# Kernel tuning notes

Measured on AMD Instinct MI355X. Metric: run time of the kernel, lower is better.

## Reference

```python
import jax, jax.numpy as jnp
import numpy as np

X_DIM, Y_DIM = 16, 8
D_MODEL, N_HEADS, N_LAYERS = 256, 8, 8
D_HEAD = D_MODEL // N_HEADS            # 32 (hidden_out_size // n_heads)
D_FF = D_HEAD * 8 * N_HEADS            # 2048 (feed_forward_dimensions)
B, S_PAST, S_FUT = 4, 1024, 512
MIN_STD = 0.01
LN_EPS = 1e-5
ATTN_EPS = 1e-6


def setup_inputs() -> dict:
    key = jax.random.key(0)
    ks = jax.random.split(key, 24)
    def nrm(k, shape, s=0.02):
        return jax.random.normal(k, shape, jnp.float32) * s
    L, d, dff = N_LAYERS, D_MODEL, D_FF
    x_size = X_DIM + Y_DIM
    return {
        "past_x": jax.random.normal(ks[0], (B, S_PAST, X_DIM), jnp.float32),
        "past_y": jax.random.normal(ks[1], (B, S_PAST, Y_DIM), jnp.float32),
        "future_x": jax.random.normal(ks[2], (B, S_FUT, X_DIM), jnp.float32),
        "enc_W": nrm(ks[3], (x_size, d)), "enc_b": jnp.zeros((d,), jnp.float32),
        "Wq": nrm(ks[4], (L, d, d)), "bq": jnp.zeros((L, d), jnp.float32),
        "Wk": nrm(ks[5], (L, d, d)), "bk": jnp.zeros((L, d), jnp.float32),
        "Wv": nrm(ks[6], (L, d, d)), "bv": jnp.zeros((L, d), jnp.float32),
        "Wo": nrm(ks[7], (L, d, d)), "bo": jnp.zeros((L, d), jnp.float32),
        "ln1_w": jnp.ones((L, d), jnp.float32), "ln1_b": jnp.zeros((L, d), jnp.float32),
        "W1": nrm(ks[8], (L, d, dff)), "b1": jnp.zeros((L, dff), jnp.float32),
        "W2": nrm(ks[9], (L, dff, d)), "b2": jnp.zeros((L, d), jnp.float32),
        "ln2_w": jnp.ones((L, d), jnp.float32), "ln2_b": jnp.zeros((L, d), jnp.float32),
        "mean_W": nrm(ks[10], (d, Y_DIM)), "mean_b": jnp.zeros((Y_DIM,), jnp.float32),
        "std_W": nrm(ks[11], (d, Y_DIM)), "std_b": jnp.zeros((Y_DIM,), jnp.float32),
    }


def _ln(x, w, b):
    m = jnp.mean(x, axis=-1, keepdims=True)
    v = jnp.var(x, axis=-1, keepdims=True)
    return (x - m) * jax.lax.rsqrt(v + LN_EPS) * w + b


def _causal_linear_attn(q, k, v):
    # q,k,v: [B, N, H, D]; phi(x) = elu(x) + 1 (fast_transformers default feature map)
    q = jax.nn.elu(q) + 1.0
    k = jax.nn.elu(k) + 1.0
    # cumulative outer-product state S_i = sum_{j<=i} phi(k_j) v_j^T : [B,N,H,D,D]
    kv = jnp.cumsum(jnp.einsum('bnhd,bnhm->bnhdm', k, v), axis=1)
    num = jnp.einsum('bnhd,bnhdm->bnhm', q, kv)
    z = jnp.einsum('bnhd,bnhd->bnh', q, jnp.cumsum(k, axis=1))
    return num / (z[..., None] + ATTN_EPS)


def _forward(past_x, past_y, future_x, enc_W, enc_b, Wq, bq, Wk, bk, Wv, bv,
             Wo, bo, ln1_w, ln1_b, W1, b1, W2, b2, ln2_w, ln2_b,
             mean_W, mean_b, std_W, std_b):
    Bz, Sf = future_x.shape[0], future_x.shape[1]
    steps = past_y.shape[1]
    # future y placeholder = last observed y, repeated
    fy = jnp.repeat(past_y[:, -1:, :], Sf, axis=1)
    context = jnp.concatenate([past_x, past_y], axis=-1)
    target = jnp.concatenate([future_x, fy], axis=-1)
    x = jax.lax.stop_gradient(jnp.concatenate([context, target], axis=1))  # .detach()
    x = x @ enc_W + enc_b                      # [B, N, D_MODEL]
    N = x.shape[1]
    for i in range(N_LAYERS):
        q = (x @ Wq[i] + bq[i]).reshape(Bz, N, N_HEADS, D_HEAD)
        k = (x @ Wk[i] + bk[i]).reshape(Bz, N, N_HEADS, D_HEAD)
        v = (x @ Wv[i] + bv[i]).reshape(Bz, N, N_HEADS, D_HEAD)
        a = _causal_linear_attn(q, k, v).reshape(Bz, N, D_MODEL)
        x = _ln(x + (a @ Wo[i] + bo[i]), ln1_w[i], ln1_b[i])   # post-norm (fast_transformers)
        y = jax.nn.relu(x @ W1[i] + b1[i]) @ W2[i] + b2[i]
        x = _ln(x + y, ln2_w[i], ln2_b[i])
    out = x[:, steps:, :]                      # keep only the target segment
    mean = out @ mean_W + mean_b
    sigma = MIN_STD + (1.0 - MIN_STD) * jax.nn.softplus(out @ std_W + std_b)
    return mean, sigma


def reference(past_x, past_y, future_x, enc_W, enc_b, Wq, bq, Wk, bk, Wv, bv,
              Wo, bo, ln1_w, ln1_b, W1, b1, W2, b2, ln2_w, ln2_b,
              mean_W, mean_b, std_W, std_b):
    return _forward(past_x, past_y, future_x, enc_W, enc_b, Wq, bq, Wk, bk,
                    Wv, bv, Wo, bo, ln1_w, ln1_b, W1, b1, W2, b2,
                    ln2_w, ln2_b, mean_W, mean_b, std_W, std_b)
```

## Files before the change

### kernel.cpp

```cpp
#include <hip/hip_runtime.h>
#include <hip/hip_bf16.h>
#include <math.h>

#define BB 4
#define SP 1024
#define SF 512
#define NN 1536
#define DD 256
#define HH 8
#define DH 32
#define DFF 2048
#define LL 8
#define TOK (BB*NN)
#define NSEG 48
#define SEGLEN 32

typedef __attribute__((ext_vector_type(8))) short bf16x8;
typedef __attribute__((ext_vector_type(4))) float f32x4;
typedef __hip_bfloat16 bf16;

__device__ __forceinline__ void gld_lds16(const void* g, void* l) {
    __builtin_amdgcn_global_load_lds(
        (const __attribute__((address_space(1))) void*)g,
        (__attribute__((address_space(3))) void*)l, 16, 0, 0);
}

__global__ __launch_bounds__(256) void wtrans_kernel(
    const float* __restrict__ src, bf16* __restrict__ dst, int K, int N)
{
    __shared__ float tile[64][65];
    int k0 = blockIdx.x*64, n0 = blockIdx.y*64;
    const float* s = src + (size_t)blockIdx.z*K*N;
    bf16* d = dst + (size_t)blockIdx.z*K*N;
    int t = threadIdx.x, c = t & 63, r4 = t >> 6;
    #pragma unroll
    for (int rr = 0; rr < 64; rr += 4)
        tile[rr+r4][c] = s[(size_t)(k0+rr+r4)*N + n0 + c];
    __syncthreads();
    #pragma unroll
    for (int rr = 0; rr < 64; rr += 4) {
        int n = rr + r4;
        d[(size_t)(n0+n)*K + k0 + c] = __float2bfloat16(tile[c][n]);
    }
}

template<int BM, bool SPLITK, bool BOUT>
__device__ __forceinline__ void gemm_core(
    const bf16* __restrict__ A, const bf16* __restrict__ Wt,
    const float* __restrict__ bias, float* __restrict__ Cf,
    bf16* __restrict__ Cb, int N, int K, int epi, int kc0, int kc1)
{
    constexpr int MI = BM/32;
    __shared__ bf16 As[BM*64];
    __shared__ bf16 Bs[128*64];
    int tid = threadIdx.x, lane = tid & 63, wid = tid >> 6;
    int m0 = blockIdx.x*BM, n0 = blockIdx.y*128;
    int wm = (wid & 1)*(BM/2), wn = (wid >> 1)*64;

    f32x4 acc[MI][4] = {};

    int rA = wid*(BM/4) + (lane >> 3);
    int rB = wid*32 + (lane >> 3);
    int c_st = (lane & 7)*8;
    const bf16* Ag = A  + (size_t)(m0 + rA)*K + c_st;
    const bf16* Bg = Wt + (size_t)(n0 + rB)*K + c_st;
    bf16* Asw = As + (wid*(BM/4))*64;
    bf16* Bsw = Bs + (wid*32)*64;

    int a_off = (wm + (lane & 15))*64 + (lane >> 4)*8;
    int b_off = (wn + (lane & 15))*64 + (lane >> 4)*8;

    for (int kc = kc0; kc < kc1; kc += 64) {
        #pragma unroll
        for (int i = 0; i < MI; i++)
            gld_lds16(Ag + (size_t)(i*8)*K + kc, Asw + (i*8)*64);
        #pragma unroll
        for (int i = 0; i < 4; i++)
            gld_lds16(Bg + (size_t)(i*8)*K + kc, Bsw + (i*8)*64);
        __syncthreads();
        #pragma unroll
        for (int ks = 0; ks < 2; ks++) {
            bf16x8 af[MI], bfr[4];
            #pragma unroll
            for (int i = 0; i < MI; i++)
                af[i] = *(const bf16x8*)(As + a_off + i*16*64 + ks*32);
            #pragma unroll
            for (int j = 0; j < 4; j++)
                bfr[j] = *(const bf16x8*)(Bs + b_off + j*16*64 + ks*32);
            #pragma unroll
            for (int i = 0; i < MI; i++)
                #pragma unroll
                for (int j = 0; j < 4; j++)
                    acc[i][j] = __builtin_amdgcn_mfma_f32_16x16x32_bf16(
                        af[i], bfr[j], acc[i][j], 0, 0, 0);
        }
        __syncthreads();
    }

    if constexpr (BOUT) {
        bf16* Ct = Bs;
        #pragma unroll
        for (int j = 0; j < 4; j++) {
            int col = wn + j*16 + (lane & 15);
            float bv = bias[n0 + col];
            #pragma unroll
            for (int i = 0; i < MI; i++) {
                #pragma unroll
                for (int r = 0; r < 4; r++) {
                    int row = wm + i*16 + (lane >> 4)*4 + r;
                    float v = acc[i][j][r] + bv;
                    if (epi == 1) v = fmaxf(v, 0.f);
                    else if (epi == 2) v = (v > 0.f) ? v + 1.f : expf(v);
                    Ct[row*128 + (col ^ (((row >> 2) & 3) << 4))] = __float2bfloat16(v);
                }
            }
        }
        __syncthreads();
        #pragma unroll
        for (int u = 0; u < 4; u++) {
            int e = tid*32 + u*8;
            int row = e >> 7, c0 = e & 127;
            bf16x8 val = *(const bf16x8*)(Ct + row*128 + (c0 ^ (((row >> 2) & 3) << 4)));
            *(bf16x8*)(Cb + (size_t)(m0 + row)*N + n0 + c0) = val;
        }
    } else {
        int col_base = n0 + wn + (lane & 15);
        int row_base = m0 + wm + (lane >> 4)*4;
        #pragma unroll
        for (int j = 0; j < 4; j++) {
            int col = col_base + j*16;
            float bv = SPLITK ? 0.f : bias[col];
            #pragma unroll
            for (int i = 0; i < MI; i++) {
                #pragma unroll
                for (int r = 0; r < 4; r++) {
                    int row = row_base + i*16 + r;
                    if (SPLITK) {
                        unsafeAtomicAdd(&Cf[(size_t)row*N + col], acc[i][j][r]);
                    } else {
                        float v = acc[i][j][r] + bv;
                        if (epi == 1) v = fmaxf(v, 0.f);
                        else if (epi == 2) v = (v > 0.f) ? v + 1.f : expf(v);
                        if (Cb) Cb[(size_t)row*N + col] = __float2bfloat16(v);
                        else    Cf[(size_t)row*N + col] = v;
                    }
                }
            }
        }
    }
}

template<int BM, bool BOUT>
__global__ __launch_bounds__(256) void mfma_gemm_kernel(
    const bf16* __restrict__ A, const bf16* __restrict__ Wt,
    const float* __restrict__ bias, float* __restrict__ Cf,
    bf16* __restrict__ Cb, int N, int K, int epi)
{
    gemm_core<BM, false, BOUT>(A, Wt, bias, Cf, Cb, N, K, epi, 0, K);
}

template<int BM>
__global__ __launch_bounds__(256) void mfma_gemm_splitk_kernel(
    const bf16* __restrict__ A, const bf16* __restrict__ Wt,
    float* __restrict__ Cf, int N, int K, int KC)
{
    int kc0 = blockIdx.z*KC;
    gemm_core<BM, true, false>(A, Wt, nullptr, Cf, nullptr, N, K, 0, kc0, kc0 + KC);
}

template<int BM>
__global__ __launch_bounds__(256) void mfma_qkv_kernel(
    const bf16* __restrict__ Xb,
    const bf16* __restrict__ Wqt, const bf16* __restrict__ Wkt, const bf16* __restrict__ Wvt,
    const float* __restrict__ bq, const float* __restrict__ bk, const float* __restrict__ bv,
    float* __restrict__ Q, float* __restrict__ K, float* __restrict__ V, int layer)
{
    int z = blockIdx.z;
    const bf16* Wt = (z == 0) ? Wqt : (z == 1) ? Wkt : Wvt;
    const float* b = (z == 0) ? bq : (z == 1) ? bk : bv;
    float* C = (z == 0) ? Q : (z == 1) ? K : V;
    gemm_core<BM, false, false>(Xb, Wt + (size_t)layer*DD*DD, b + (size_t)layer*DD,
                                C, nullptr, DD, DD, (z == 2) ? 0 : 2, 0, DD);
}

__global__ __launch_bounds__(256) void encode_kernel(
    const float* __restrict__ px, const float* __restrict__ py,
    const float* __restrict__ fx, const float* __restrict__ encW,
    const float* __restrict__ encb, float* __restrict__ X, bf16* __restrict__ Xb)
{
    int tok = blockIdx.x;
    int t = threadIdx.x;
    int b = tok / NN, n = tok % NN;
    __shared__ float in[24];
    if (t < 16) {
        in[t] = (n < SP) ? px[((size_t)b*SP + n)*16 + t]
                         : fx[((size_t)b*SF + (n - SP))*16 + t];
    } else if (t < 24) {
        int j = t - 16;
        in[t] = (n < SP) ? py[((size_t)b*SP + n)*8 + j]
                         : py[((size_t)b*SP + (SP-1))*8 + j];
    }
    __syncthreads();
    float acc = encb[t];
    #pragma unroll
    for (int j = 0; j < 24; j++) acc = fmaf(in[j], encW[j*DD + t], acc);
    X[(size_t)tok*DD + t] = acc;
    Xb[(size_t)tok*DD + t] = __float2bfloat16(acc);
}

__global__ __launch_bounds__(256) void attnA_kernel(
    const float* __restrict__ K, const float* __restrict__ V,
    float* __restrict__ SegS, float* __restrict__ SegZ)
{
    int bid = blockIdx.x;
    int seg = bid % NSEG; int bh = bid / NSEG;
    int h = bh & 7, b = bh >> 3;
    int t = threadIdx.x;
    int d = t & 31, mg = t >> 5, m0 = mg*4;
    int tok0 = b*NN + seg*SEGLEN;
    const float* Kp = K + (size_t)tok0*DD + h*DH;
    const float* Vp = V + (size_t)tok0*DD + h*DH;
    float a0=0,a1=0,a2=0,a3=0, ks=0;
    #pragma unroll 4
    for (int i = 0; i < SEGLEN; i++) {
        float kd = Kp[(size_t)i*DD + d];
        float4 vv = *(const float4*)(Vp + (size_t)i*DD + m0);
        a0 = fmaf(kd, vv.x, a0); a1 = fmaf(kd, vv.y, a1);
        a2 = fmaf(kd, vv.z, a2); a3 = fmaf(kd, vv.w, a3);
        ks += kd;
    }
    float4 o = {a0, a1, a2, a3};
    *(float4*)(SegS + ((size_t)bid*32 + d)*32 + m0) = o;
    if (mg == 0) SegZ[(size_t)bid*32 + d] = ks;
}

__global__ __launch_bounds__(256) void attnA2_kernel(
    float* __restrict__ SegS, float* __restrict__ SegZ)
{
    int bh = blockIdx.x, y = blockIdx.y, t = threadIdx.x;
    int e = y*256 + t;
    float* p = SegS + (size_t)bh*NSEG*1024 + e;
    float v[NSEG];
    #pragma unroll
    for (int s = 0; s < NSEG; s++) v[s] = p[(size_t)s*1024];
    float run = 0.f;
    #pragma unroll
    for (int s = 0; s < NSEG; s++) {
        p[(size_t)s*1024] = run;
        run += v[s];
    }
    if (y == 0 && t < 32) {
        float* pz = SegZ + (size_t)bh*NSEG*32 + t;
        float vz[NSEG];
        #pragma unroll
        for (int s = 0; s < NSEG; s++) vz[s] = pz[(size_t)s*32];
        float runz = 0.f;
        #pragma unroll
        for (int s = 0; s < NSEG; s++) {
            pz[(size_t)s*32] = runz;
            runz += vz[s];
        }
    }
}

__global__ __launch_bounds__(256) void attnB_kernel(
    const float* __restrict__ Q, const float* __restrict__ K, const float* __restrict__ V,
    const float* __restrict__ SegS, const float* __restrict__ SegZ,
    bf16* __restrict__ A)
{
    int wid = threadIdx.x >> 6;
    int lane = threadIdx.x & 63;
    int bid = blockIdx.x*4 + wid;
    int seg = bid % NSEG; int bh = bid / NSEG;
    int h = bh & 7, b = bh >> 3;
    int m = lane & 31, dh = lane >> 5, dh16 = dh*16;
    int tok0 = b*NN + seg*SEGLEN;

    __shared__ float qs[4][SEGLEN][32], ksm[4][SEGLEN][32], vs[4][SEGLEN][32];
    const float* Qp = Q + (size_t)tok0*DD + h*DH;
    const float* Kp = K + (size_t)tok0*DD + h*DH;
    const float* Vp = V + (size_t)tok0*DD + h*DH;
    #pragma unroll
    for (int f = lane; f < SEGLEN*8; f += 64) {
        int r = f >> 3, c = (f & 7)*4;
        *(float4*)&qs[wid][r][c]  = *(const float4*)(Qp + (size_t)r*DD + c);
        *(float4*)&ksm[wid][r][c] = *(const float4*)(Kp + (size_t)r*DD + c);
        *(float4*)&vs[wid][r][c]  = *(const float4*)(Vp + (size_t)r*DD + c);
    }
    __syncthreads();

    float kv[16], kss[16];
    const float* Pp = SegS + (size_t)bid*1024;
    const float* Zp = SegZ + (size_t)bid*32;
    #pragma unroll
    for (int j = 0; j < 16; j++) {
        kv[j]  = Pp[(dh16 + j)*32 + m];
        kss[j] = Zp[dh16 + j];
    }

    bf16* Ap = A + (size_t)tok0*DD + h*DH;
    for (int i = 0; i < SEGLEN; i++) {
        float qv[16], kk[16];
        #pragma unroll
        for (int c = 0; c < 4; c++) {
            float4 t4 = *(const float4*)&qs[wid][i][dh16 + 4*c];
            qv[4*c] = t4.x; qv[4*c+1] = t4.y; qv[4*c+2] = t4.z; qv[4*c+3] = t4.w;
            float4 k4 = *(const float4*)&ksm[wid][i][dh16 + 4*c];
            kk[4*c] = k4.x; kk[4*c+1] = k4.y; kk[4*c+2] = k4.z; kk[4*c+3] = k4.w;
        }
        float vm = vs[wid][i][m];
        #pragma unroll
        for (int j = 0; j < 16; j++) {
            kv[j] = fmaf(kk[j], vm, kv[j]);
            kss[j] += kk[j];
        }
        float p0=0,p1=0,p2=0,p3=0,z0=0,z1=0,z2=0,z3=0;
        #pragma unroll
        for (int j = 0; j < 4; j++) {
            p0 = fmaf(qv[j],     kv[j],     p0);
            p1 = fmaf(qv[4+j],   kv[4+j],   p1);
            p2 = fmaf(qv[8+j],   kv[8+j],   p2);
            p3 = fmaf(qv[12+j],  kv[12+j],  p3);
            z0 = fmaf(qv[j],     kss[j],    z0);
            z1 = fmaf(qv[4+j],   kss[4+j],  z1);
            z2 = fmaf(qv[8+j],   kss[8+j],  z2);
            z3 = fmaf(qv[12+j],  kss[12+j], z3);
        }
        float nump = (p0+p1)+(p2+p3);
        float zp   = (z0+z1)+(z2+z3);
        nump += __shfl_xor(nump, 32, 64);
        zp   += __shfl_xor(zp,   32, 64);
        if (dh == 0) Ap[(size_t)i*DD + m] = __float2bfloat16(nump / (zp + 1e-6f));
    }
}

__global__ __launch_bounds__(256) void resid_ln_kernel(
    const float* __restrict__ Xin, const float* __restrict__ G,
    const float* __restrict__ gb,
    const float* __restrict__ w, const float* __restrict__ b,
    float* __restrict__ Xout, bf16* __restrict__ Xbout)
{
    int tok = blockIdx.x, t = threadIdx.x;
    size_t idx = (size_t)tok*DD + t;
    float v = Xin[idx] + G[idx] + (gb ? gb[t] : 0.f);
    float s = v, s2 = v*v;
    #pragma unroll
    for (int off = 32; off >= 1; off >>= 1) {
        s  += __shfl_xor(s,  off, 64);
        s2 += __shfl_xor(s2, off, 64);
    }
    __shared__ float ps[4], ps2[4];
    int wid = t >> 6;
    if ((t & 63) == 0) { ps[wid] = s; ps2[wid] = s2; }
    __syncthreads();
    float S  = ps[0] + ps[1] + ps[2] + ps[3];
    float S2 = ps2[0] + ps2[1] + ps2[2] + ps2[3];
    float mean = S * (1.f/256.f);
    float var  = S2 * (1.f/256.f) - mean*mean;
    float o = (v - mean) * rsqrtf(var + 1e-5f) * w[t] + b[t];
    Xout[idx] = o;
    Xbout[idx] = __float2bfloat16(o);
}

__global__ __launch_bounds__(256) void head_kernel(
    const float* __restrict__ X,
    const float* __restrict__ meanW, const float* __restrict__ meanB,
    const float* __restrict__ stdW,  const float* __restrict__ stdB,
    float* __restrict__ out)
{
    int wv = threadIdx.x >> 6;
    int lane = threadIdx.x & 63;
    int idx = blockIdx.x*4 + wv;
    int b = idx / SF, i = idx % SF;
    const float* row = X + ((size_t)(b*NN + SP + i))*DD;
    __shared__ float xs[4][DD];
    *(float4*)&xs[wv][lane*4] = *(const float4*)(row + lane*4);
    __syncthreads();

    int j = lane & 7;
    int which = (lane >> 3) & 1;
    int seg = lane >> 4;
    const float* W = which ? stdW : meanW;
    float p = 0.f;
    #pragma unroll 16
    for (int d = seg*64; d < seg*64 + 64; d++) p = fmaf(xs[wv][d], W[d*8 + j], p);
    p += __shfl_xor(p, 16, 64);
    p += __shfl_xor(p, 32, 64);
    if (lane < 16) {
        if (which == 0) {
            out[((size_t)b*SF + i)*8 + j] = p + meanB[j];
        } else {
            float s = p + stdB[j];
            float sp = fmaxf(s, 0.f) + log1pf(expf(-fabsf(s)));
            out[(size_t)BB*SF*8 + ((size_t)b*SF + i)*8 + j] = 0.01f + 0.99f*sp;
        }
    }
}

extern "C" void kernel_launch(void* const* d_in, const int* in_sizes, int n_in,
                              void* d_out, int out_size, void* d_ws, size_t ws_size,
                              hipStream_t stream)
{
    (void)in_sizes; (void)n_in; (void)out_size; (void)ws_size;
    const float* past_x   = (const float*)d_in[0];
    const float* past_y   = (const float*)d_in[1];
    const float* future_x = (const float*)d_in[2];
    const float* enc_W    = (const float*)d_in[3];
    const float* enc_b    = (const float*)d_in[4];
    const float* Wq       = (const float*)d_in[5];
    const float* bq       = (const float*)d_in[6];
    const float* Wk       = (const float*)d_in[7];
    const float* bk       = (const float*)d_in[8];
    const float* Wv       = (const float*)d_in[9];
    const float* bv       = (const float*)d_in[10];
    const float* Wo       = (const float*)d_in[11];
    const float* bo       = (const float*)d_in[12];
    const float* ln1_w    = (const float*)d_in[13];
    const float* ln1_b    = (const float*)d_in[14];
    const float* W1       = (const float*)d_in[15];
    const float* b1       = (const float*)d_in[16];
    const float* W2       = (const float*)d_in[17];
    const float* b2       = (const float*)d_in[18];
    const float* ln2_w    = (const float*)d_in[19];
    const float* ln2_b    = (const float*)d_in[20];
    const float* mean_W   = (const float*)d_in[21];
    const float* mean_b   = (const float*)d_in[22];
    const float* std_W    = (const float*)d_in[23];
    const float* std_b    = (const float*)d_in[24];
    float* out = (float*)d_out;

    char* base = (char*)d_ws;
    size_t off = 0;
    float* X  = (float*)(base + off); off += (size_t)TOK*DD*4;
    bf16* Xb  = (bf16*)(base + off);  off += (size_t)TOK*DD*2;
    bf16* Hb  = (bf16*)(base + off);  off += (size_t)TOK*DFF*2;
    float* Qb = (float*)Hb;
    float* Kb = Qb + (size_t)TOK*DD;
    float* Vb = Kb + (size_t)TOK*DD;
    bf16* Ab  = (bf16*)(base + off);  off += (size_t)TOK*DD*2;
    float* G  = (float*)(base + off); off += (size_t)TOK*DD*4;
    float* SegS = (float*)(base + off); off += (size_t)BB*HH*NSEG*1024*4;
    float* SegZ = (float*)(base + off); off += (size_t)BB*HH*NSEG*32*4;
    bf16* Wqt = (bf16*)(base + off); off += (size_t)LL*DD*DD*2;
    bf16* Wkt = (bf16*)(base + off); off += (size_t)LL*DD*DD*2;
    bf16* Wvt = (bf16*)(base + off); off += (size_t)LL*DD*DD*2;
    bf16* Wot = (bf16*)(base + off); off += (size_t)LL*DD*DD*2;
    bf16* W1t = (bf16*)(base + off); off += (size_t)LL*DD*DFF*2;
    bf16* W2t = (bf16*)(base + off); off += (size_t)LL*DFF*DD*2;

    wtrans_kernel<<<dim3(4, 4, LL),  256, 0, stream>>>(Wq, Wqt, DD, DD);
    wtrans_kernel<<<dim3(4, 4, LL),  256, 0, stream>>>(Wk, Wkt, DD, DD);
    wtrans_kernel<<<dim3(4, 4, LL),  256, 0, stream>>>(Wv, Wvt, DD, DD);
    wtrans_kernel<<<dim3(4, 4, LL),  256, 0, stream>>>(Wo, Wot, DD, DD);
    wtrans_kernel<<<dim3(4, 32, LL), 256, 0, stream>>>(W1, W1t, DD, DFF);
    wtrans_kernel<<<dim3(32, 4, LL), 256, 0, stream>>>(W2, W2t, DFF, DD);

    encode_kernel<<<TOK, 256, 0, stream>>>(past_x, past_y, future_x, enc_W, enc_b, X, Xb);

    for (int l = 0; l < LL; l++) {
        mfma_qkv_kernel<32><<<dim3(TOK/32, 2, 3), 256, 0, stream>>>(
            Xb, Wqt, Wkt, Wvt, bq, bk, bv, Qb, Kb, Vb, l);
        attnA_kernel<<<BB*HH*NSEG, 256, 0, stream>>>(Kb, Vb, SegS, SegZ);
        attnA2_kernel<<<dim3(BB*HH, 4), 256, 0, stream>>>(SegS, SegZ);
        attnB_kernel<<<BB*HH*NSEG/4, 256, 0, stream>>>(Qb, Kb, Vb, SegS, SegZ, Ab);
        mfma_gemm_kernel<32, false><<<dim3(TOK/32, 2), 256, 0, stream>>>(
            Ab, Wot + (size_t)l*DD*DD, bo + (size_t)l*DD, G, nullptr, DD, DD, 0);
        resid_ln_kernel<<<TOK, 256, 0, stream>>>(
            X, G, nullptr, ln1_w + l*DD, ln1_b + l*DD, X, Xb);
        mfma_gemm_kernel<64, true><<<dim3(TOK/64, DFF/128), 256, 0, stream>>>(
            Xb, W1t + (size_t)l*DD*DFF, b1 + (size_t)l*DFF, nullptr, Hb, DFF, DD, 1);
        hipMemsetAsync(G, 0, (size_t)TOK*DD*4, stream);
        mfma_gemm_splitk_kernel<64><<<dim3(TOK/64, 2, 4), 256, 0, stream>>>(
            Hb, W2t + (size_t)l*DFF*DD, G, DD, DFF, DFF/4);
        resid_ln_kernel<<<TOK, 256, 0, stream>>>(
            X, G, b2 + (size_t)l*DD, ln2_w + l*DD, ln2_b + l*DD, X, Xb);
    }

    head_kernel<<<(BB*SF)/4, 256, 0, stream>>>(X, mean_W, mean_b, std_W, std_b, out);
}
```

Baseline: 1.141 ms.

## Fuse Wo GEMM with residual LayerNorm and replace split-K atomics with slices

Adds a wo_ln_kernel in which each block computes a full 256-wide row tile of the attention output projection, adds the bias and residual, and applies LayerNorm in-register. This removes one GEMM launch, one LN launch and the fp32 G round trip. The W2 split-K GEMM now writes four separate partial slices instead of atomically adding into a zeroed buffer, so the memset and the atomics go away, and the LN kernel sums the slices. The four small weight transposes are merged into one launch. The cost is a larger workspace, extra reads of the partial slices, and fewer blocks for the Wo GEMM (TOK/32 instead of 2x that).

```diff
diff --git a/kernel.cpp b/kernel.cpp
--- a/kernel.cpp
+++ b/kernel.cpp
@@ -25,13 +25,11 @@
         (__attribute__((address_space(3))) void*)l, 16, 0, 0);
 }
 
-__global__ __launch_bounds__(256) void wtrans_kernel(
-    const float* __restrict__ src, bf16* __restrict__ dst, int K, int N)
+__device__ __forceinline__ void wtrans_tile(
+    const float* __restrict__ s, bf16* __restrict__ d, int K, int N,
+    int k0, int n0)
 {
     __shared__ float tile[64][65];
-    int k0 = blockIdx.x*64, n0 = blockIdx.y*64;
-    const float* s = src + (size_t)blockIdx.z*K*N;
-    bf16* d = dst + (size_t)blockIdx.z*K*N;
     int t = threadIdx.x, c = t & 63, r4 = t >> 6;
     #pragma unroll
     for (int rr = 0; rr < 64; rr += 4)
@@ -44,7 +42,28 @@
     }
 }
 
-template<int BM, bool SPLITK, bool BOUT>
+__global__ __launch_bounds__(256) void wtrans_kernel(
+    const float* __restrict__ src, bf16* __restrict__ dst, int K, int N)
+{
+    wtrans_tile(src + (size_t)blockIdx.z*K*N, dst + (size_t)blockIdx.z*K*N,
+                K, N, blockIdx.x*64, blockIdx.y*64);
+}
+
+__global__ __launch_bounds__(256) void wtrans4_kernel(
+    const float* __restrict__ Wq, const float* __restrict__ Wk,
+    const float* __restrict__ Wv, const float* __restrict__ Wo,
+    bf16* __restrict__ Wqt, bf16* __restrict__ Wkt,
+    bf16* __restrict__ Wvt, bf16* __restrict__ Wot)
+{
+    int z = blockIdx.z, which = z >> 3, l = z & 7;
+    const float* s = (which == 0 ? Wq : which == 1 ? Wk : which == 2 ? Wv : Wo)
+                     + (size_t)l*DD*DD;
+    bf16* d = (which == 0 ? Wqt : which == 1 ? Wkt : which == 2 ? Wvt : Wot)
+              + (size_t)l*DD*DD;
+    wtrans_tile(s, d, DD, DD, blockIdx.x*64, blockIdx.y*64);
+}
+
+template<int BM, bool SLICE, bool BOUT>
 __device__ __forceinline__ void gemm_core(
     const bf16* __restrict__ A, const bf16* __restrict__ Wt,
     const float* __restrict__ bias, float* __restrict__ Cf,
@@ -129,14 +148,14 @@
         #pragma unroll
         for (int j = 0; j < 4; j++) {
             int col = col_base + j*16;
-            float bv = SPLITK ? 0.f : bias[col];
+            float bv = SLICE ? 0.f : bias[col];
             #pragma unroll
             for (int i = 0; i < MI; i++) {
                 #pragma unroll
                 for (int r = 0; r < 4; r++) {
                     int row = row_base + i*16 + r;
-                    if (SPLITK) {
-                        unsafeAtomicAdd(&Cf[(size_t)row*N + col], acc[i][j][r]);
+                    if (SLICE) {
+                        Cf[(size_t)row*N + col] = acc[i][j][r];
                     } else {
                         float v = acc[i][j][r] + bv;
                         if (epi == 1) v = fmaxf(v, 0.f);
@@ -160,12 +179,13 @@
 }
 
 template<int BM>
-__global__ __launch_bounds__(256) void mfma_gemm_splitk_kernel(
+__global__ __launch_bounds__(256) void mfma_gemm_slicek_kernel(
     const bf16* __restrict__ A, const bf16* __restrict__ Wt,
     float* __restrict__ Cf, int N, int K, int KC)
 {
     int kc0 = blockIdx.z*KC;
-    gemm_core<BM, true, false>(A, Wt, nullptr, Cf, nullptr, N, K, 0, kc0, kc0 + KC);
+    gemm_core<BM, true, false>(A, Wt, nullptr, Cf + (size_t)blockIdx.z*TOK*N,
+                               nullptr, N, K, 0, kc0, kc0 + KC);
 }
 
 template<int BM>
@@ -181,6 +201,109 @@
     float* C = (z == 0) ? Q : (z == 1) ? K : V;
     gemm_core<BM, false, false>(Xb, Wt + (size_t)layer*DD*DD, b + (size_t)layer*DD,
                                 C, nullptr, DD, DD, (z == 2) ? 0 : 2, 0, DD);
+}
+
+__global__ __launch_bounds__(256) void wo_ln_kernel(
+    const bf16* __restrict__ A, const bf16* __restrict__ Wt,
+    const float* __restrict__ bias,
+    const float* __restrict__ lnw, const float* __restrict__ lnb,
+    float* __restrict__ X, bf16* __restrict__ Xb)
+{
+    __shared__ bf16 As[32*64];
+    __shared__ bf16 Bs[256*64];
+    __shared__ float red[2][4][32];
+    int tid = threadIdx.x, lane = tid & 63, wid = tid >> 6;
+    int m0 = blockIdx.x*32;
+    int wn = wid*64;
+
+    f32x4 acc[2][4] = {};
+
+    int rA = wid*8 + (lane >> 3);
+    int c_st = (lane & 7)*8;
+    const bf16* Ag = A + (size_t)(m0 + rA)*DD + c_st;
+    const bf16* Bg = Wt + (size_t)(wn + (lane >> 3))*DD + c_st;
+    bf16* Asw = As + (wid*8)*64;
+    bf16* Bsw = Bs + wn*64;
+
+    int a_off = (lane & 15)*64 + (lane >> 4)*8;
+    int b_off = (wn + (lane & 15))*64 + (lane >> 4)*8;
+
+    for (int kc = 0; kc < DD; kc += 64) {
+        gld_lds16(Ag + kc, Asw);
+        #pragma unroll
+        for (int i = 0; i < 8; i++)
+            gld_lds16(Bg + (size_t)(i*8)*DD + kc, Bsw + (i*8)*64);
+        __syncthreads();
+        #pragma unroll
+        for (int ks = 0; ks < 2; ks++) {
+            bf16x8 af[2], bfr[4];
+            af[0] = *(const bf16x8*)(As + a_off + ks*32);
+            af[1] = *(const bf16x8*)(As + a_off + 16*64 + ks*32);
+            #pragma unroll
+            for (int j = 0; j < 4; j++)
+                bfr[j] = *(const bf16x8*)(Bs + b_off + j*16*64 + ks*32);
+            #pragma unroll
+            for (int i = 0; i < 2; i++)
+                #pragma unroll
+                for (int j = 0; j < 4; j++)
+                    acc[i][j] = __builtin_amdgcn_mfma_f32_16x16x32_bf16(
+                        af[i], bfr[j], acc[i][j], 0, 0, 0);
+        }
+        __syncthreads();
+    }
+
+    #pragma unroll
+    for (int j = 0; j < 4; j++) {
+        int c = wn + j*16 + (lane & 15);
+        float bv = bias[c];
+        #pragma unroll
+        for (int i = 0; i < 2; i++) {
+            int row = m0 + i*16 + (lane >> 4)*4;
+            #pragma unroll
+            for (int r = 0; r < 4; r++)
+                acc[i][j][r] += bv + X[(size_t)(row + r)*DD + c];
+        }
+    }
+    #pragma unroll
+    for (int i = 0; i < 2; i++) {
+        #pragma unroll
+        for (int r = 0; r < 4; r++) {
+            float s  = (acc[i][0][r] + acc[i][1][r]) + (acc[i][2][r] + acc[i][3][r]);
+            float s2 = (acc[i][0][r]*acc[i][0][r] + acc[i][1][r]*acc[i][1][r])
+                     + (acc[i][2][r]*acc[i][2][r] + acc[i][3][r]*acc[i][3][r]);
+            #pragma unroll
+            for (int off = 1; off < 16; off <<= 1) {
+                s  += __shfl_xor(s,  off, 64);
+                s2 += __shfl_xor(s2, off, 64);
+            }
+            if ((lane & 15) == 0) {
+                int rloc = i*16 + (lane >> 4)*4 + r;
+                red[0][wid][rloc] = s;
+                red[1][wid][rloc] = s2;
+            }
+        }
+    }
+    __syncthreads();
+    #pragma unroll
+    for (int i = 0; i < 2; i++) {
+        #pragma unroll
+        for (int r = 0; r < 4; r++) {
+            int rloc = i*16 + (lane >> 4)*4 + r;
+            float S  = (red[0][0][rloc] + red[0][1][rloc]) + (red[0][2][rloc] + red[0][3][rloc]);
+            float S2 = (red[1][0][rloc] + red[1][1][rloc]) + (red[1][2][rloc] + red[1][3][rloc]);
+            float mean = S * (1.f/256.f);
+            float var  = S2 * (1.f/256.f) - mean*mean;
+            float rs = rsqrtf(var + 1e-5f);
+            #pragma unroll
+            for (int j = 0; j < 4; j++) {
+                int c = wn + j*16 + (lane & 15);
+                float o = (acc[i][j][r] - mean) * rs * lnw[c] + lnb[c];
+                size_t idx = (size_t)(m0 + rloc)*DD + c;
+                X[idx] = o;
+                Xb[idx] = __float2bfloat16(o);
+            }
+        }
+    }
 }
 
 __global__ __launch_bounds__(256) void encode_kernel(
@@ -334,15 +457,17 @@
     }
 }
 
-__global__ __launch_bounds__(256) void resid_ln_kernel(
-    const float* __restrict__ Xin, const float* __restrict__ G,
+__global__ __launch_bounds__(256) void resid_ln4_kernel(
+    const float* __restrict__ Xin, const float* __restrict__ G4,
     const float* __restrict__ gb,
     const float* __restrict__ w, const float* __restrict__ b,
     float* __restrict__ Xout, bf16* __restrict__ Xbout)
 {
+    const size_t SZ = (size_t)TOK*DD;
     int tok = blockIdx.x, t = threadIdx.x;
     size_t idx = (size_t)tok*DD + t;
-    float v = Xin[idx] + G[idx] + (gb ? gb[t] : 0.f);
+    float v = Xin[idx] + gb[t]
+            + ((G4[idx] + G4[SZ + idx]) + (G4[2*SZ + idx] + G4[3*SZ + idx]));
     float s = v, s2 = v*v;
     #pragma unroll
     for (int off = 32; off >= 1; off >>= 1) {
@@ -438,7 +563,7 @@
     float* Kb = Qb + (size_t)TOK*DD;
     float* Vb = Kb + (size_t)TOK*DD;
     bf16* Ab  = (bf16*)(base + off);  off += (size_t)TOK*DD*2;
-    float* G  = (float*)(base + off); off += (size_t)TOK*DD*4;
+    float* G4 = (float*)(base + off); off += (size_t)4*TOK*DD*4;
     float* SegS = (float*)(base + off); off += (size_t)BB*HH*NSEG*1024*4;
     float* SegZ = (float*)(base + off); off += (size_t)BB*HH*NSEG*32*4;
     bf16* Wqt = (bf16*)(base + off); off += (size_t)LL*DD*DD*2;
@@ -448,10 +573,8 @@
     bf16* W1t = (bf16*)(base + off); off += (size_t)LL*DD*DFF*2;
     bf16* W2t = (bf16*)(base + off); off += (size_t)LL*DFF*DD*2;
 
-    wtrans_kernel<<<dim3(4, 4, LL),  256, 0, stream>>>(Wq, Wqt, DD, DD);
-    wtrans_kernel<<<dim3(4, 4, LL),  256, 0, stream>>>(Wk, Wkt, DD, DD);
-    wtrans_kernel<<<dim3(4, 4, LL),  256, 0, stream>>>(Wv, Wvt, DD, DD);
-    wtrans_kernel<<<dim3(4, 4, LL),  256, 0, stream>>>(Wo, Wot, DD, DD);
+    wtrans4_kernel<<<dim3(4, 4, 4*LL), 256, 0, stream>>>(
+        Wq, Wk, Wv, Wo, Wqt, Wkt, Wvt, Wot);
     wtrans_kernel<<<dim3(4, 32, LL), 256, 0, stream>>>(W1, W1t, DD, DFF);
     wtrans_kernel<<<dim3(32, 4, LL), 256, 0, stream>>>(W2, W2t, DFF, DD);
 
@@ -463,17 +586,15 @@
         attnA_kernel<<<BB*HH*NSEG, 256, 0, stream>>>(Kb, Vb, SegS, SegZ);
         attnA2_kernel<<<dim3(BB*HH, 4), 256, 0, stream>>>(SegS, SegZ);
         attnB_kernel<<<BB*HH*NSEG/4, 256, 0, stream>>>(Qb, Kb, Vb, SegS, SegZ, Ab);
-        mfma_gemm_kernel<32, false><<<dim3(TOK/32, 2), 256, 0, stream>>>(
-            Ab, Wot + (size_t)l*DD*DD, bo + (size_t)l*DD, G, nullptr, DD, DD, 0);
-        resid_ln_kernel<<<TOK, 256, 0, stream>>>(
-            X, G, nullptr, ln1_w + l*DD, ln1_b + l*DD, X, Xb);
+        wo_ln_kernel<<<TOK/32, 256, 0, stream>>>(
+            Ab, Wot + (size_t)l*DD*DD, bo + (size_t)l*DD,
+            ln1_w + l*DD, ln1_b + l*DD, X, Xb);
         mfma_gemm_kernel<64, true><<<dim3(TOK/64, DFF/128), 256, 0, stream>>>(
             Xb, W1t + (size_t)l*DD*DFF, b1 + (size_t)l*DFF, nullptr, Hb, DFF, DD, 1);
-        hipMemsetAsync(G, 0, (size_t)TOK*DD*4, stream);
-        mfma_gemm_splitk_kernel<64><<<dim3(TOK/64, 2, 4), 256, 0, stream>>>(
-            Hb, W2t + (size_t)l*DFF*DD, G, DD, DFF, DFF/4);
-        resid_ln_kernel<<<TOK, 256, 0, stream>>>(
-            X, G, b2 + (size_t)l*DD, ln2_w + l*DD, ln2_b + l*DD, X, Xb);
+        mfma_gemm_slicek_kernel<64><<<dim3(TOK/64, 2, 4), 256, 0, stream>>>(
+            Hb, W2t + (size_t)l*DFF*DD, G4, DD, DFF, DFF/4);
+        resid_ln4_kernel<<<TOK, 256, 0, stream>>>(
+            X, G4, b2 + (size_t)l*DD, ln2_w + l*DD, ln2_b + l*DD, X, Xb);
     }
 
     head_kernel<<<(BB*SF)/4, 256, 0, stream>>>(X, mean_W, mean_b, std_W, std_b, out);
```

After: 993.9 us. -12.9%, faster.
